# Optimization experiments

Measured on AMD Instinct MI355X. Metric: run time of the kernel, lower is better.

The kernel has to match this reference:

```python
import jax, jax.numpy as jnp
import numpy as np

B, L, P, D = 512, 32, 256, 2


def hungarian(cost):
    """Min-cost assignment on an [n,n] numpy cost matrix (rows=pred, cols=target).
    Returns col[row]: target index assigned to each pred row (same as scipy
    linear_sum_assignment col_ind). Jonker-Volgenant style augmenting path."""
    n = cost.shape[0]
    INF = 1e18
    u = np.zeros(n + 1)
    v = np.zeros(n + 1)
    p = np.zeros(n + 1, dtype=np.int64)
    way = np.zeros(n + 1, dtype=np.int64)
    for i in range(1, n + 1):
        p[0] = i
        j0 = 0
        minv = np.full(n + 1, INF)
        used = np.zeros(n + 1, dtype=bool)
        while True:
            used[j0] = True
            i0 = p[j0]
            free = ~used[1:]
            cur = cost[i0 - 1, :] - u[i0] - v[1:]
            upd = free & (cur < minv[1:])
            m1 = minv[1:]
            m1[upd] = cur[upd]
            w1 = way[1:]
            w1[upd] = j0
            mfree = np.where(free, m1, INF)
            j1 = int(np.argmin(mfree)) + 1
            delta = mfree[j1 - 1]
            u[p[used]] += delta
            v[used] -= delta
            m1[free] -= delta
            j0 = j1
            if p[j0] == 0:
                break
        while j0:
            j1 = way[j0]
            p[j0] = p[j1]
            j0 = j1
    col = np.zeros(n, dtype=np.int64)
    for j in range(1, n + 1):
        col[p[j] - 1] = j - 1
    return col


def match_targets_np(pred_flat, tgt_flat, n_lines):
    """pred_flat/tgt_flat: np [B, L, P*D]; n_lines: np int [B].
    Replicates match_lines_sequence: Hungarian on pairwise squared L2 over the
    first n valid lines; unmatched rows stay zero (they are masked in the loss)."""
    out = np.zeros_like(pred_flat)
    for b in range(pred_flat.shape[0]):
        n = int(n_lines[b])
        if n == 1:
            out[b] = tgt_flat[b]
            continue
        pr = pred_flat[b, :n]
        tg = tgt_flat[b, :n]
        cost = ((pr[:, None, :] - tg[None, :, :]) ** 2).sum(-1)  # [pred, target]
        col = hungarian(cost)
        out[b, :n] = tgt_flat[b][col]
    return out


def setup_inputs() -> dict:
    key = jax.random.key(0)
    ks = jax.random.split(key, 5)
    point_pos_pred = jax.random.normal(ks[0], (B, L, P, D), jnp.float32)
    target_pos = jax.random.normal(ks[1], (B, L, P, D), jnp.float32)
    # probabilities in (0,1), bounded away from 0 so -log is finite
    line_prob_pred = jax.random.uniform(ks[2], (B, L, 2), jnp.float32) * 0.9 + 0.05
    n_lines = jax.random.randint(ks[3], (B,), 1, L + 1)
    line_masks = (jnp.arange(L)[None, :] < n_lines[:, None]).astype(jnp.float32)
    clf_line = jax.random.randint(ks[4], (B, L), 0, 2).astype(jnp.int32)
    point_masks = (line_masks[:, :, None] * jnp.ones((1, 1, P), jnp.float32))
    return {
        "point_pos_pred": point_pos_pred,
        "line_prob_pred": line_prob_pred,
        "target_pos": target_pos,
        "line_masks": line_masks,
        "clf_line": clf_line,
        "point_masks": point_masks,
    }


def reference(point_pos_pred, line_prob_pred, target_pos, line_masks, clf_line, point_masks):
    # --- Hungarian matching (host-side, non-differentiable, as in the original) ---
    pp = np.asarray(point_pos_pred).reshape(B, L, P * D)
    tp = np.asarray(target_pos).reshape(B, L, P * D)
    n_lines = np.asarray(line_masks).sum(axis=1).astype(np.int64)
    matched = jnp.asarray(match_targets_np(pp, tp, n_lines)).reshape(B, L, P, D)
    # --- masked MSE over (point, dim) ---
    sq = jnp.sum((point_pos_pred - matched) ** 2, axis=-1) * point_masks  # [B,L,P]
    mask_mse = jnp.sum(sq) / jnp.sum(point_masks)
    # --- masked NLL on line existence probabilities ---
    neg_log = -jnp.log(line_prob_pred).reshape(-1, 2)        # [B*L, 2]
    picked = jnp.take_along_axis(neg_log, clf_line.reshape(-1, 1), axis=1)
    clf_loss = jnp.sum(picked * line_masks.reshape(-1, 1)) / jnp.sum(line_masks)
    return (mask_mse, clf_loss)
```

## Files before the change

kernel.cpp:

```cpp
#include <hip/hip_runtime.h>
#include <cstdint>
#include <cstddef>

#define NB 512
#define NL 32
#define KD 512
#define HKD 256

__device__ __forceinline__ int swz_off(int row, int ch) {
  int csw = (ch & ~15) | ((ch ^ (row >> 1)) & 15);
  return row * HKD + csw * 4;
}

__global__ __launch_bounds__(256, 2)
void cost_kernel(const float* __restrict__ pred, const float* __restrict__ tgt,
                 float* __restrict__ cost_g) {
  __shared__ float smem[16384];
  const int b = blockIdx.x;
  const int tid = threadIdx.x;
  float* predH = smem;
  float* tgtH  = smem + 8192;

  const int w = tid >> 6, l = tid & 63;
  const int ti = l >> 3, tj = l & 7;
  float acc[4][4];
#pragma unroll
  for (int a = 0; a < 4; ++a)
#pragma unroll
    for (int c2 = 0; c2 < 4; ++c2) acc[a][c2] = 0.f;

  for (int hp = 0; hp < 2; ++hp) {
    __syncthreads();
    const size_t base = (size_t)b * (NL * KD) + (size_t)hp * HKD;
#pragma unroll
    for (int it = 0; it < 8; ++it) {
      int chunk = tid + it * 256;
      int row = chunk >> 6, ch = chunk & 63;
      const float4 pv = *reinterpret_cast<const float4*>(pred + base + (size_t)row * KD + ch * 4);
      const float4 tv = *reinterpret_cast<const float4*>(tgt  + base + (size_t)row * KD + ch * 4);
      int off = swz_off(row, ch);
      *reinterpret_cast<float4*>(predH + off) = pv;
      *reinterpret_cast<float4*>(tgtH  + off) = tv;
    }
    __syncthreads();
#pragma unroll
    for (int c0 = 0; c0 < 16; ++c0) {
      const int c = (w << 4) + c0;
      float4 pr[4], tg[4];
#pragma unroll
      for (int r = 0; r < 4; ++r) {
        pr[r] = *reinterpret_cast<const float4*>(predH + swz_off(4 * ti + r, c));
        tg[r] = *reinterpret_cast<const float4*>(tgtH  + swz_off(4 * tj + r, c));
      }
#pragma unroll
      for (int a = 0; a < 4; ++a)
#pragma unroll
        for (int c2 = 0; c2 < 4; ++c2) {
          float d;
          d = pr[a].x - tg[c2].x; acc[a][c2] += d * d;
          d = pr[a].y - tg[c2].y; acc[a][c2] += d * d;
          d = pr[a].z - tg[c2].z; acc[a][c2] += d * d;
          d = pr[a].w - tg[c2].w; acc[a][c2] += d * d;
        }
    }
  }
  __syncthreads();
#pragma unroll
  for (int a = 0; a < 4; ++a)
#pragma unroll
    for (int c2 = 0; c2 < 4; ++c2)
      smem[w * 1024 + (ti & 3) + 4 * tj + 32 * a + 128 * c2 + 512 * (ti >> 2)] = acc[a][c2];
  __syncthreads();
  const int ti2 = tid >> 5, a2 = (tid >> 3) & 3, tj2 = tid & 7;
  float ov[4];
#pragma unroll
  for (int k = 0; k < 4; ++k) {
    int ad = (ti2 & 3) + 4 * tj2 + 32 * a2 + 128 * k + 512 * (ti2 >> 2);
    ov[k] = (smem[ad] + smem[ad + 1024]) + (smem[ad + 2048] + smem[ad + 3072]);
  }
  float4 o4 = make_float4(ov[0], ov[1], ov[2], ov[3]);
  *reinterpret_cast<float4*>(cost_g + (size_t)b * 1024 + tid * 4) = o4;
}

__device__ __forceinline__ float readlane_f(float x, int lane) {
  return __int_as_float(__builtin_amdgcn_readlane(__float_as_int(x), lane));
}
__device__ __forceinline__ int readlane_i(int x, int lane) {
  return __builtin_amdgcn_readlane(x, lane);
}

template<int CTRL, int RM>
__device__ __forceinline__ float dppmin(float x) {
  int m = __builtin_amdgcn_update_dpp(__float_as_int(x), __float_as_int(x), CTRL, RM, 0xf, false);
  return fminf(x, __int_as_float(m));
}
__device__ __forceinline__ float wave_min32_bcast(float x) {
  x = dppmin<0xB1, 0xf>(x);
  x = dppmin<0x4E, 0xf>(x);
  x = dppmin<0x124, 0xf>(x);
  x = dppmin<0x128, 0xf>(x);
  x = dppmin<0x142, 0xa>(x);
  return readlane_f(x, 31);
}

__global__ __launch_bounds__(64)
void hung_kernel(const float* __restrict__ cost_g,
                 const float* __restrict__ prob,
                 const float* __restrict__ lmask,
                 const int* __restrict__ clf,
                 float* __restrict__ part) {
  __shared__ float cs[1024];
  const int b = blockIdx.x;
  const int lane = threadIdx.x;

  {
    const float4* src = reinterpret_cast<const float4*>(cost_g + (size_t)b * 1024);
    float4* dst = reinterpret_cast<float4*>(cs);
#pragma unroll
    for (int k = 0; k < 4; ++k) dst[lane + 64 * k] = src[lane + 64 * k];
  }

  float lm = (lane < 32) ? lmask[b * 32 + lane] : 0.f;
  const int n = __popcll(__ballot(lm > 0.5f));
  float clfpart = 0.f;
  if (lane < 32 && lm > 0.5f) {
    int cc = clf[b * 32 + lane];
    clfpart = -logf(prob[(size_t)(b * 32 + lane) * 2 + cc]);
  }
  __syncthreads();

  const float FINF = 1e30f;
  const bool activecol = (lane < n);
  const int cl = lane & 31;

  float u_r = 0.f, v_j = 0.f;
  int p_j = -1;

  for (int ri = 0; ri < n; ++ri) {
    int i0 = ri;
    bool usedc = false;
    bool usedr = (lane == ri);
    float rowv = cs[i0 * 32 + cl];
    while (true) {
      float key = rowv - v_j;
      bool act = activecol && !usedc;
      float m = act ? key : FINF;
      float u0 = readlane_f(u_r, i0);
      float mn = wave_min32_bcast(m);
      uint64_t tie = __ballot(m == mn);
      int j1 = __ffsll((unsigned long long)tie) - 1;
      int pj1 = readlane_i(p_j, j1);
      int i0n = pj1 < 0 ? 0 : pj1;
      float rowv_n = cs[i0n * 32 + cl];
      float delta = mn - u0;
      if (usedr) u_r += delta;
      if (usedc) v_j -= delta;
      if (pj1 < 0) {
        if (lane == j1) p_j = ri;
        break;
      }
      usedc = usedc || (lane == j1);
      i0 = pj1;
      usedr = usedr || (lane == i0);
      rowv = rowv_n;
    }
  }

  int pj = p_j < 0 ? 0 : p_j;
  float a = activecol ? cs[pj * 32 + cl] : 0.f;
#pragma unroll
  for (int off = 32; off; off >>= 1) {
    a += __shfl_xor(a, off);
    clfpart += __shfl_xor(clfpart, off);
  }
  if (lane == 0) {
    part[b * 3 + 0] = a;
    part[b * 3 + 1] = clfpart;
    part[b * 3 + 2] = (float)n;
  }
}

__global__ void finalize_kernel(const float* __restrict__ part, float* __restrict__ out) {
  const int lane = threadIdx.x;
  double cs = 0.0, ls = 0.0, ns = 0.0;
  for (int i = lane; i < NB; i += 64) {
    cs += (double)part[i * 3 + 0];
    ls += (double)part[i * 3 + 1];
    ns += (double)part[i * 3 + 2];
  }
#pragma unroll
  for (int off = 32; off; off >>= 1) {
    cs += __shfl_xor(cs, off);
    ls += __shfl_xor(ls, off);
    ns += __shfl_xor(ns, off);
  }
  if (lane == 0) {
    out[0] = (float)(cs / (ns * 256.0));
    out[1] = (float)(ls / ns);
  }
}

extern "C" void kernel_launch(void* const* d_in, const int* in_sizes, int n_in,
                              void* d_out, int out_size, void* d_ws, size_t ws_size,
                              hipStream_t stream) {
  const float* pred = (const float*)d_in[0];
  const float* prob = (const float*)d_in[1];
  const float* tgt  = (const float*)d_in[2];
  const float* lm   = (const float*)d_in[3];
  const int*   clf  = (const int*)d_in[4];

  float* cost_g = (float*)d_ws;
  float* part   = cost_g + (size_t)NB * 1024;

  cost_kernel<<<NB, 256, 0, stream>>>(pred, tgt, cost_g);
  hung_kernel<<<NB, 64, 0, stream>>>(cost_g, prob, lm, clf, part);
  finalize_kernel<<<1, 64, 0, stream>>>(part, (float*)d_out);
}
```

Before: 73.07 us.

## Fuse cost, Hungarian and finalize kernels into one with last-block reduction

Merges the cost-matrix kernel, the per-batch Hungarian kernel and the finalize kernel into one launch. Blocks grow to 512 threads, and the cost matrix is reduced across eight waves in shared memory, so it no longer goes through global memory. A global atomic counter lets the last block do the final reduction. This removes two kernel launches and the global round-trip of the cost matrix, but adds a memset and leaves 7 of 8 waves idle during the serial Hungarian phase, which may hurt occupancy overlap.

```diff
diff --git a/kernel.cpp b/kernel.cpp
--- a/kernel.cpp
+++ b/kernel.cpp
@@ -12,9 +12,36 @@
   return row * HKD + csw * 4;
 }
 
-__global__ __launch_bounds__(256, 2)
-void cost_kernel(const float* __restrict__ pred, const float* __restrict__ tgt,
-                 float* __restrict__ cost_g) {
+__device__ __forceinline__ float readlane_f(float x, int lane) {
+  return __int_as_float(__builtin_amdgcn_readlane(__float_as_int(x), lane));
+}
+__device__ __forceinline__ int readlane_i(int x, int lane) {
+  return __builtin_amdgcn_readlane(x, lane);
+}
+
+template<int CTRL, int RM>
+__device__ __forceinline__ float dppmin(float x) {
+  int m = __builtin_amdgcn_update_dpp(__float_as_int(x), __float_as_int(x), CTRL, RM, 0xf, false);
+  return fminf(x, __int_as_float(m));
+}
+__device__ __forceinline__ float wave_min32_bcast(float x) {
+  x = dppmin<0xB1, 0xf>(x);
+  x = dppmin<0x4E, 0xf>(x);
+  x = dppmin<0x124, 0xf>(x);
+  x = dppmin<0x128, 0xf>(x);
+  x = dppmin<0x142, 0xa>(x);
+  return readlane_f(x, 31);
+}
+
+__global__ __launch_bounds__(512, 4)
+void fused_kernel(const float* __restrict__ pred,
+                  const float* __restrict__ prob,
+                  const float* __restrict__ tgt,
+                  const float* __restrict__ lmask,
+                  const int* __restrict__ clf,
+                  float* __restrict__ part,
+                  unsigned int* __restrict__ counter,
+                  float* __restrict__ out) {
   __shared__ float smem[16384];
   const int b = blockIdx.x;
   const int tid = threadIdx.x;
@@ -33,8 +60,8 @@
     __syncthreads();
     const size_t base = (size_t)b * (NL * KD) + (size_t)hp * HKD;
 #pragma unroll
-    for (int it = 0; it < 8; ++it) {
-      int chunk = tid + it * 256;
+    for (int it = 0; it < 4; ++it) {
+      int chunk = tid + it * 512;
       int row = chunk >> 6, ch = chunk & 63;
       const float4 pv = *reinterpret_cast<const float4*>(pred + base + (size_t)row * KD + ch * 4);
       const float4 tv = *reinterpret_cast<const float4*>(tgt  + base + (size_t)row * KD + ch * 4);
@@ -44,8 +71,8 @@
     }
     __syncthreads();
 #pragma unroll
-    for (int c0 = 0; c0 < 16; ++c0) {
-      const int c = (w << 4) + c0;
+    for (int c0 = 0; c0 < 8; ++c0) {
+      const int c = (w << 3) + c0;
       float4 pr[4], tg[4];
 #pragma unroll
       for (int r = 0; r < 4; ++r) {
@@ -66,59 +93,25 @@
   }
   __syncthreads();
 #pragma unroll
-  for (int a = 0; a < 4; ++a)
-#pragma unroll
-    for (int c2 = 0; c2 < 4; ++c2)
-      smem[w * 1024 + (ti & 3) + 4 * tj + 32 * a + 128 * c2 + 512 * (ti >> 2)] = acc[a][c2];
+  for (int a = 0; a < 4; ++a) {
+    float4 v = make_float4(acc[a][0], acc[a][1], acc[a][2], acc[a][3]);
+    *reinterpret_cast<float4*>(&smem[w * 1024 + (4 * ti + a) * 32 + 4 * tj]) = v;
+  }
   __syncthreads();
-  const int ti2 = tid >> 5, a2 = (tid >> 3) & 3, tj2 = tid & 7;
-  float ov[4];
-#pragma unroll
-  for (int k = 0; k < 4; ++k) {
-    int ad = (ti2 & 3) + 4 * tj2 + 32 * a2 + 128 * k + 512 * (ti2 >> 2);
-    ov[k] = (smem[ad] + smem[ad + 1024]) + (smem[ad + 2048] + smem[ad + 3072]);
-  }
-  float4 o4 = make_float4(ov[0], ov[1], ov[2], ov[3]);
-  *reinterpret_cast<float4*>(cost_g + (size_t)b * 1024 + tid * 4) = o4;
-}
-
-__device__ __forceinline__ float readlane_f(float x, int lane) {
-  return __int_as_float(__builtin_amdgcn_readlane(__float_as_int(x), lane));
-}
-__device__ __forceinline__ int readlane_i(int x, int lane) {
-  return __builtin_amdgcn_readlane(x, lane);
-}
-
-template<int CTRL, int RM>
-__device__ __forceinline__ float dppmin(float x) {
-  int m = __builtin_amdgcn_update_dpp(__float_as_int(x), __float_as_int(x), CTRL, RM, 0xf, false);
-  return fminf(x, __int_as_float(m));
-}
-__device__ __forceinline__ float wave_min32_bcast(float x) {
-  x = dppmin<0xB1, 0xf>(x);
-  x = dppmin<0x4E, 0xf>(x);
-  x = dppmin<0x124, 0xf>(x);
-  x = dppmin<0x128, 0xf>(x);
-  x = dppmin<0x142, 0xa>(x);
-  return readlane_f(x, 31);
-}
-
-__global__ __launch_bounds__(64)
-void hung_kernel(const float* __restrict__ cost_g,
-                 const float* __restrict__ prob,
-                 const float* __restrict__ lmask,
-                 const int* __restrict__ clf,
-                 float* __restrict__ part) {
-  __shared__ float cs[1024];
-  const int b = blockIdx.x;
-  const int lane = threadIdx.x;
-
   {
-    const float4* src = reinterpret_cast<const float4*>(cost_g + (size_t)b * 1024);
-    float4* dst = reinterpret_cast<float4*>(cs);
-#pragma unroll
-    for (int k = 0; k < 4; ++k) dst[lane + 64 * k] = src[lane + 64 * k];
-  }
+    float2 s = make_float2(0.f, 0.f);
+#pragma unroll
+    for (int w2 = 0; w2 < 8; ++w2) {
+      float2 p = *reinterpret_cast<const float2*>(&smem[w2 * 1024 + 2 * tid]);
+      s.x += p.x; s.y += p.y;
+    }
+    *reinterpret_cast<float2*>(&smem[8192 + 2 * tid]) = s;
+  }
+  __syncthreads();
+
+  if (tid >= 64) return;
+  const float* cs = smem + 8192;
+  const int lane = tid;
 
   float lm = (lane < 32) ? lmask[b * 32 + lane] : 0.f;
   const int n = __popcll(__ballot(lm > 0.5f));
@@ -127,7 +120,6 @@
     int cc = clf[b * 32 + lane];
     clfpart = -logf(prob[(size_t)(b * 32 + lane) * 2 + cc]);
   }
-  __syncthreads();
 
   const float FINF = 1e30f;
   const bool activecol = (lane < n);
@@ -178,25 +170,30 @@
     part[b * 3 + 1] = clfpart;
     part[b * 3 + 2] = (float)n;
   }
-}
-
-__global__ void finalize_kernel(const float* __restrict__ part, float* __restrict__ out) {
-  const int lane = threadIdx.x;
-  double cs = 0.0, ls = 0.0, ns = 0.0;
-  for (int i = lane; i < NB; i += 64) {
-    cs += (double)part[i * 3 + 0];
-    ls += (double)part[i * 3 + 1];
-    ns += (double)part[i * 3 + 2];
-  }
-#pragma unroll
-  for (int off = 32; off; off >>= 1) {
-    cs += __shfl_xor(cs, off);
-    ls += __shfl_xor(ls, off);
-    ns += __shfl_xor(ns, off);
-  }
-  if (lane == 0) {
-    out[0] = (float)(cs / (ns * 256.0));
-    out[1] = (float)(ls / ns);
+
+  __threadfence();
+  unsigned int t = 0;
+  if (lane == 0) t = atomicAdd(counter, 1u);
+  t = (unsigned int)__shfl((int)t, 0);
+  if (t == NB - 1u) {
+    __threadfence();
+    volatile const float* vp = part;
+    double csum = 0.0, lsum = 0.0, nsum = 0.0;
+    for (int i = lane; i < NB; i += 64) {
+      csum += (double)vp[i * 3 + 0];
+      lsum += (double)vp[i * 3 + 1];
+      nsum += (double)vp[i * 3 + 2];
+    }
+#pragma unroll
+    for (int off = 32; off; off >>= 1) {
+      csum += __shfl_xor(csum, off);
+      lsum += __shfl_xor(lsum, off);
+      nsum += __shfl_xor(nsum, off);
+    }
+    if (lane == 0) {
+      out[0] = (float)(csum / (nsum * 256.0));
+      out[1] = (float)(lsum / nsum);
+    }
   }
 }
 
@@ -209,10 +206,10 @@
   const float* lm   = (const float*)d_in[3];
   const int*   clf  = (const int*)d_in[4];
 
-  float* cost_g = (float*)d_ws;
-  float* part   = cost_g + (size_t)NB * 1024;
-
-  cost_kernel<<<NB, 256, 0, stream>>>(pred, tgt, cost_g);
-  hung_kernel<<<NB, 64, 0, stream>>>(cost_g, prob, lm, clf, part);
-  finalize_kernel<<<1, 64, 0, stream>>>(part, (float*)d_out);
-}
+  float* part = (float*)d_ws;
+  unsigned int* counter = (unsigned int*)((char*)d_ws + 8192);
+
+  hipMemsetAsync(counter, 0, sizeof(unsigned int), stream);
+  fused_kernel<<<NB, 512, 0, stream>>>(pred, prob, tgt, lm, clf, part, counter,
+                                       (float*)d_out);
+}
```

New measurement: 116.2 us. 59.1% more time.

## Split cost matrix K dimension across two blocks per batch, sum partials in hung kernel

Applied to the files above, without the earlier changes.

The cost kernel now launches two blocks per batch element, each covering half of the 512-wide feature dimension in two 128-wide passes. Each block uses half the shared memory and the launch bounds ask for higher occupancy. The Hungarian kernel reads and sums the two partial cost matrices when loading them. This raises parallelism on the 256-CU device and shrinks per-block LDS use, at the price of twice the intermediate writes and reads plus more global workspace.

```diff
diff --git a/kernel.cpp b/kernel.cpp
--- a/kernel.cpp
+++ b/kernel.cpp
@@ -5,21 +5,24 @@
 #define NB 512
 #define NL 32
 #define KD 512
-#define HKD 256
-
-__device__ __forceinline__ int swz_off(int row, int ch) {
+#define KSLAB 256
+#define PASS 128
+
+__device__ __forceinline__ int swz128(int row, int ch) {
   int csw = (ch & ~15) | ((ch ^ (row >> 1)) & 15);
-  return row * HKD + csw * 4;
-}
-
-__global__ __launch_bounds__(256, 2)
+  return row * PASS + csw * 4;
+}
+
+__global__ __launch_bounds__(256, 4)
 void cost_kernel(const float* __restrict__ pred, const float* __restrict__ tgt,
-                 float* __restrict__ cost_g) {
-  __shared__ float smem[16384];
-  const int b = blockIdx.x;
+                 float* __restrict__ cost_part) {
+  __shared__ float smem[8192];
+  const int bid = blockIdx.x;
+  const int b  = bid >> 1;
+  const int ks = (bid & 1) * KSLAB;
   const int tid = threadIdx.x;
   float* predH = smem;
-  float* tgtH  = smem + 8192;
+  float* tgtH  = smem + 4096;
 
   const int w = tid >> 6, l = tid & 63;
   const int ti = l >> 3, tj = l & 7;
@@ -31,26 +34,26 @@
 
   for (int hp = 0; hp < 2; ++hp) {
     __syncthreads();
-    const size_t base = (size_t)b * (NL * KD) + (size_t)hp * HKD;
-#pragma unroll
-    for (int it = 0; it < 8; ++it) {
+    const size_t base = (size_t)b * (NL * KD) + ks + hp * PASS;
+#pragma unroll
+    for (int it = 0; it < 4; ++it) {
       int chunk = tid + it * 256;
-      int row = chunk >> 6, ch = chunk & 63;
+      int row = chunk >> 5, ch = chunk & 31;
       const float4 pv = *reinterpret_cast<const float4*>(pred + base + (size_t)row * KD + ch * 4);
       const float4 tv = *reinterpret_cast<const float4*>(tgt  + base + (size_t)row * KD + ch * 4);
-      int off = swz_off(row, ch);
+      int off = swz128(row, ch);
       *reinterpret_cast<float4*>(predH + off) = pv;
       *reinterpret_cast<float4*>(tgtH  + off) = tv;
     }
     __syncthreads();
 #pragma unroll
-    for (int c0 = 0; c0 < 16; ++c0) {
-      const int c = (w << 4) + c0;
+    for (int c0 = 0; c0 < 8; ++c0) {
+      const int c = (w << 3) + c0;
       float4 pr[4], tg[4];
 #pragma unroll
       for (int r = 0; r < 4; ++r) {
-        pr[r] = *reinterpret_cast<const float4*>(predH + swz_off(4 * ti + r, c));
-        tg[r] = *reinterpret_cast<const float4*>(tgtH  + swz_off(4 * tj + r, c));
+        pr[r] = *reinterpret_cast<const float4*>(predH + swz128(4 * ti + r, c));
+        tg[r] = *reinterpret_cast<const float4*>(tgtH  + swz128(4 * tj + r, c));
       }
 #pragma unroll
       for (int a = 0; a < 4; ++a)
@@ -79,7 +82,7 @@
     ov[k] = (smem[ad] + smem[ad + 1024]) + (smem[ad + 2048] + smem[ad + 3072]);
   }
   float4 o4 = make_float4(ov[0], ov[1], ov[2], ov[3]);
-  *reinterpret_cast<float4*>(cost_g + (size_t)b * 1024 + tid * 4) = o4;
+  *reinterpret_cast<float4*>(cost_part + (size_t)bid * 1024 + tid * 4) = o4;
 }
 
 __device__ __forceinline__ float readlane_f(float x, int lane) {
@@ -104,7 +107,7 @@
 }
 
 __global__ __launch_bounds__(64)
-void hung_kernel(const float* __restrict__ cost_g,
+void hung_kernel(const float* __restrict__ cost_part,
                  const float* __restrict__ prob,
                  const float* __restrict__ lmask,
                  const int* __restrict__ clf,
@@ -114,10 +117,15 @@
   const int lane = threadIdx.x;
 
   {
-    const float4* src = reinterpret_cast<const float4*>(cost_g + (size_t)b * 1024);
-    float4* dst = reinterpret_cast<float4*>(cs);
-#pragma unroll
-    for (int k = 0; k < 4; ++k) dst[lane + 64 * k] = src[lane + 64 * k];
+    const float4* c0p = reinterpret_cast<const float4*>(cost_part + (size_t)(2 * b) * 1024);
+    const float4* c1p = reinterpret_cast<const float4*>(cost_part + (size_t)(2 * b + 1) * 1024);
+    float4* cs4 = reinterpret_cast<float4*>(cs);
+#pragma unroll
+    for (int k = 0; k < 4; ++k) {
+      int i = lane + 64 * k;
+      float4 x = c0p[i], y = c1p[i];
+      cs4[i] = make_float4(x.x + y.x, x.y + y.y, x.z + y.z, x.w + y.w);
+    }
   }
 
   float lm = (lane < 32) ? lmask[b * 32 + lane] : 0.f;
@@ -209,10 +217,10 @@
   const float* lm   = (const float*)d_in[3];
   const int*   clf  = (const int*)d_in[4];
 
-  float* cost_g = (float*)d_ws;
-  float* part   = cost_g + (size_t)NB * 1024;
-
-  cost_kernel<<<NB, 256, 0, stream>>>(pred, tgt, cost_g);
-  hung_kernel<<<NB, 64, 0, stream>>>(cost_g, prob, lm, clf, part);
+  float* cost_part = (float*)d_ws;
+  float* part = cost_part + (size_t)1024 * 1024;
+
+  cost_kernel<<<NB * 2, 256, 0, stream>>>(pred, tgt, cost_part);
+  hung_kernel<<<NB, 64, 0, stream>>>(cost_part, prob, lm, clf, part);
   finalize_kernel<<<1, 64, 0, stream>>>(part, (float*)d_out);
 }
```

Result: slower. 110.3 us (+50.9%).
